# Kernel optimization log

Hardware: AMD Instinct MI355X
Metric: run time of the kernel (lower is better)

Reference implementation:

```python
import jax, jax.numpy as jnp
import numpy as np

INPUT_SIZE = 1024
OUTPUT_SIZE = 1024
HEADS = 8
FREQ = 10000.0
NEG_INF = -1e9


def absolute_position(T, d, freq):
    # AP[p, 2i] = sin(p / freq^(2i/d)); AP[p, 2i+1] = cos(...). T assumed even.
    pos = jnp.arange(T, dtype=jnp.float32)[:, None]          # [T, 1]
    i = jnp.arange(T // 2, dtype=jnp.float32)[None, :]       # [1, T//2]
    angle = pos / (freq ** (2.0 * i / d))                    # [T, T//2]
    return jnp.stack([jnp.sin(angle), jnp.cos(angle)], axis=-1).reshape(T, T)


def setup_inputs() -> dict:
    key = jax.random.key(0)
    k_x, k_m, k_q, k_k, k_v, k_o = jax.random.split(key, 6)
    bs, n = 4, 2048
    dh = OUTPUT_SIZE // HEADS
    s_in = 1.0 / np.sqrt(INPUT_SIZE)
    s_out = 1.0 / np.sqrt(OUTPUT_SIZE)
    return {
        "x": jax.random.normal(k_x, (bs, n, INPUT_SIZE), dtype=jnp.float32),
        "mask": jax.random.randint(k_m, (bs, n), 0, 2, dtype=jnp.int32),
        # torch Linear weight layout: [out_features, in_features], stacked per head -> [H, dh, D]
        "Wq": jax.random.uniform(k_q, (HEADS, dh, INPUT_SIZE), jnp.float32, -s_in, s_in),
        "Wk": jax.random.uniform(k_k, (HEADS, dh, INPUT_SIZE), jnp.float32, -s_in, s_in),
        "Wv": jax.random.uniform(k_v, (HEADS, dh, INPUT_SIZE), jnp.float32, -s_in, s_in),
        "Wout": jax.random.uniform(k_o, (INPUT_SIZE, OUTPUT_SIZE), jnp.float32, -s_out, s_out),
    }


def reference(x, mask, Wq, Wk, Wv, Wout):
    bs, n, d = x.shape
    # per-head projections (no bias): [b, h, n, dh]
    Q = jnp.einsum('bnd,hed->bhne', x, Wq)
    K = jnp.einsum('bnd,hed->bhne', x, Wk)
    V = jnp.einsum('bnd,hed->bhne', x, Wv)
    # unscaled scores, as in the original module
    energies = jnp.einsum('bhqe,bhke->bhqk', Q, K)             # [b, h, n, n]
    AP = absolute_position(n, d, FREQ)                         # [n, n]
    energies = energies + AP
    m = mask.astype(bool)
    attn_mask = m[:, None, :, None] & m[:, None, None, :]      # [b, 1, n, n]
    energies = jnp.where(attn_mask, energies, NEG_INF)
    A = jax.nn.softmax(energies, axis=-1)                      # [b, h, n, n]
    # original computes (V^T @ A)^T == A^T @ V  (note transposed attention)
    y = jnp.einsum('bhji,bhje->bhie', A, V)                    # [b, h, n, dh]
    y = y.transpose(0, 2, 1, 3).reshape(bs, n, -1)             # concat heads -> [b, n, D]
    out = jnp.einsum('bnd,od->bno', y, Wout)
    return out, A[:, -1]  # original returns last head's att_weights
```

## Files before the change

### kernel.cpp

```cpp
#include <hip/hip_runtime.h>
#include <math.h>

#define BS_ 4
#define N_  2048
#define D_  1024
#define H_  8
#define DH_ 128

typedef __attribute__((ext_vector_type(8))) short short8;
typedef __attribute__((ext_vector_type(4))) short short4_t;
typedef __attribute__((ext_vector_type(4))) float float4_t;
typedef unsigned short u16;

__device__ __forceinline__ u16 f2bf(float f) {
    union { float f; unsigned u; } v; v.f = f;
    unsigned r = v.u + 0x7FFFu + ((v.u >> 16) & 1u);
    return (u16)(r >> 16);
}
__device__ __forceinline__ float bf2f(u16 h) {
    union { unsigned u; float f; } v; v.u = ((unsigned)h) << 16;
    return v.f;
}
__device__ __forceinline__ void split4(float a, float b, float c, float d,
                                       short4_t* hi, short4_t* lo) {
    u16 h0 = f2bf(a), h1 = f2bf(b), h2 = f2bf(c), h3 = f2bf(d);
    (*hi)[0] = (short)h0; (*hi)[1] = (short)h1; (*hi)[2] = (short)h2; (*hi)[3] = (short)h3;
    (*lo)[0] = (short)f2bf(a - bf2f(h0));
    (*lo)[1] = (short)f2bf(b - bf2f(h1));
    (*lo)[2] = (short)f2bf(c - bf2f(h2));
    (*lo)[3] = (short)f2bf(d - bf2f(h3));
}

__device__ __forceinline__ void gl_lds16(const void* g, void* l) {
    __builtin_amdgcn_global_load_lds(
        (const __attribute__((address_space(1))) unsigned int*)g,
        (__attribute__((address_space(3))) unsigned int*)l,
        16, 0, 0);
}

__global__ void apt_kernel(unsigned int* __restrict__ APtw) {
    int idx = blockIdx.x * 256 + threadIdx.x;
    int i = idx >> 10;
    int jw = idx & 1023;
    int u = i >> 1;
    float ex = exp2f(-(float)u * (13.287712379549449f / 512.0f));
    float a0 = (float)(2 * jw) * ex;
    float a1 = (float)(2 * jw + 1) * ex;
    float v0, v1;
    if (i & 1) { v0 = cosf(a0); v1 = cosf(a1); }
    else       { v0 = sinf(a0); v1 = sinf(a1); }
    APtw[(size_t)i * (N_ / 2) + jw] = (unsigned)f2bf(v0) | ((unsigned)f2bf(v1) << 16);
}

__global__ void split_kernel(const float* __restrict__ x,
                             const float* __restrict__ Wq, const float* __restrict__ Wk,
                             const float* __restrict__ Wv, const float* __restrict__ Wo,
                             u16* __restrict__ Xhi, u16* __restrict__ Xlo,
                             u16* __restrict__ Whi, u16* __restrict__ Wlo,
                             u16* __restrict__ Wvhi, u16* __restrict__ Wohi) {
    int i = blockIdx.x * 256 + threadIdx.x;
    const float* src; u16 *dhi, *dlo; size_t off;
    if (i < 2097152)      { src = x  + 4*(size_t)i;             dhi = Xhi;  dlo = Xlo;  off = 4*(size_t)i; }
    else if (i < 2359296) { size_t j = i - 2097152; src = Wq + 4*j; dhi = Whi; dlo = Wlo; off = 4*j; }
    else if (i < 2621440) { size_t j = i - 2359296; src = Wk + 4*j; dhi = Whi; dlo = Wlo; off = 1048576 + 4*j; }
    else if (i < 2883584) { size_t j = i - 2621440; src = Wv + 4*j; dhi = Wvhi; dlo = nullptr; off = 4*j; }
    else                  { size_t j = i - 2883584; src = Wo + 4*j; dhi = Wohi; dlo = nullptr; off = 4*j; }
    float4 v = *(const float4*)src;
    short4_t hi, lo;
    split4(v.x, v.y, v.z, v.w, &hi, &lo);
    *(short4_t*)(dhi + off) = hi;
    if (dlo) *(short4_t*)(dlo + off) = lo;
}

__global__ __launch_bounds__(256, 4) void qk_gemm(
    const u16* __restrict__ Xhi, const u16* __restrict__ Xlo,
    const u16* __restrict__ Whi, const u16* __restrict__ Wlo,
    u16* __restrict__ Qhi, u16* __restrict__ Qlo,
    u16* __restrict__ Khi, u16* __restrict__ Klo)
{
    const int mt = blockIdx.x;
    const int nt = blockIdx.y;
    const int tid = threadIdx.x, wave = tid >> 6, lane = tid & 63;
    const int quad = lane >> 4, l16 = lane & 15;

    __shared__ __align__(16) u16 sA[2][128 * 32];
    __shared__ __align__(16) u16 sB[2][128 * 32];

    const int srow = lane >> 2;
    const int scol = (lane & 3) * 8;
    const size_t aoff = ((size_t)(mt * 128) + srow) * 1024 + scol;
    const size_t boff = ((size_t)(nt * 128) + srow) * 1024 + scol;
    const int r0 = wave * 16, r1 = 64 + wave * 16;

    float4_t acc[2][8];
#pragma unroll
    for (int i = 0; i < 2; ++i)
#pragma unroll
        for (int j = 0; j < 8; ++j) acc[i][j] = (float4_t)(0.f);

    for (int kt = 0; kt < 32; ++kt) {
        __syncthreads();
        const int kc0 = kt * 32;
        gl_lds16(Xhi + aoff + (size_t)r0 * 1024 + kc0, &sA[0][r0 * 32]);
        gl_lds16(Xhi + aoff + (size_t)r1 * 1024 + kc0, &sA[0][r1 * 32]);
        gl_lds16(Xlo + aoff + (size_t)r0 * 1024 + kc0, &sA[1][r0 * 32]);
        gl_lds16(Xlo + aoff + (size_t)r1 * 1024 + kc0, &sA[1][r1 * 32]);
        gl_lds16(Whi + boff + (size_t)r0 * 1024 + kc0, &sB[0][r0 * 32]);
        gl_lds16(Whi + boff + (size_t)r1 * 1024 + kc0, &sB[0][r1 * 32]);
        gl_lds16(Wlo + boff + (size_t)r0 * 1024 + kc0, &sB[1][r0 * 32]);
        gl_lds16(Wlo + boff + (size_t)r1 * 1024 + kc0, &sB[1][r1 * 32]);
        __syncthreads();

#pragma unroll
        for (int t = 0; t < 3; ++t) {
            const u16* As = sA[t == 2 ? 1 : 0];
            const u16* Bs = sB[t == 1 ? 1 : 0];
            short8 afr[2];
#pragma unroll
            for (int mi = 0; mi < 2; ++mi)
                afr[mi] = *(const short8*)(As + (wave * 32 + mi * 16 + l16) * 32 + quad * 8);
#pragma unroll
            for (int ne = 0; ne < 8; ++ne) {
                short8 bfr = *(const short8*)(Bs + (ne * 16 + l16) * 32 + quad * 8);
#pragma unroll
                for (int mi = 0; mi < 2; ++mi)
                    acc[mi][ne] = __builtin_amdgcn_mfma_f32_16x16x32_bf16(afr[mi], bfr, acc[mi][ne], 0, 0, 0);
            }
        }
    }

    const int b = mt >> 4, q0 = (mt & 15) * 128;
    const bool isQ = (nt < 8);
    u16* Hi = isQ ? Qhi : Khi;
    u16* Lo = isQ ? Qlo : Klo;
    const int h = isQ ? nt : nt - 8;
    const size_t base = (size_t)(b * 8 + h) * N_ * DH_;
#pragma unroll
    for (int mi = 0; mi < 2; ++mi)
#pragma unroll
        for (int ne = 0; ne < 8; ++ne)
#pragma unroll
            for (int r = 0; r < 4; ++r) {
                int q = q0 + wave * 32 + mi * 16 + quad * 4 + r;
                int e = ne * 16 + l16;
                float v = acc[mi][ne][r];
                u16 hv = f2bf(v);
                Hi[base + (size_t)q * DH_ + e] = hv;
                Lo[base + (size_t)q * DH_ + e] = f2bf(v - bf2f(hv));
            }
}

__global__ __launch_bounds__(256, 4) void v_gemm(
    const u16* __restrict__ Wvhi, const u16* __restrict__ Xhi,
    u16* __restrict__ VT)
{
    const int qt = blockIdx.x;
    const int bh = blockIdx.y;
    const int b = bh >> 3, h = bh & 7;
    const int tid = threadIdx.x, wave = tid >> 6, lane = tid & 63;
    const int quad = lane >> 4, l16 = lane & 15;

    __shared__ __align__(16) u16 sA[128 * 32];
    __shared__ __align__(16) u16 sB[128 * 32];

    const int srow = lane >> 2, scol = (lane & 3) * 8;
    const size_t aoff = ((size_t)(h * 128) + srow) * 1024 + scol;
    const size_t boff = ((size_t)(b * N_ + qt * 128) + srow) * 1024 + scol;
    const int r0 = wave * 16, r1 = 64 + wave * 16;

    float4_t acc[2][8];
#pragma unroll
    for (int i = 0; i < 2; ++i)
#pragma unroll
        for (int j = 0; j < 8; ++j) acc[i][j] = (float4_t)(0.f);

    for (int kt = 0; kt < 32; ++kt) {
        __syncthreads();
        const int kc0 = kt * 32;
        gl_lds16(Wvhi + aoff + (size_t)r0 * 1024 + kc0, &sA[r0 * 32]);
        gl_lds16(Wvhi + aoff + (size_t)r1 * 1024 + kc0, &sA[r1 * 32]);
        gl_lds16(Xhi  + boff + (size_t)r0 * 1024 + kc0, &sB[r0 * 32]);
        gl_lds16(Xhi  + boff + (size_t)r1 * 1024 + kc0, &sB[r1 * 32]);
        __syncthreads();

        short8 afr[2];
#pragma unroll
        for (int mi = 0; mi < 2; ++mi)
            afr[mi] = *(const short8*)(sA + (wave * 32 + mi * 16 + l16) * 32 + quad * 8);
#pragma unroll
        for (int ne = 0; ne < 8; ++ne) {
            short8 bfr = *(const short8*)(sB + (ne * 16 + l16) * 32 + quad * 8);
#pragma unroll
            for (int mi = 0; mi < 2; ++mi)
                acc[mi][ne] = __builtin_amdgcn_mfma_f32_16x16x32_bf16(afr[mi], bfr, acc[mi][ne], 0, 0, 0);
        }
    }

    u16* Cg = VT + (size_t)bh * DH_ * N_;
#pragma unroll
    for (int mi = 0; mi < 2; ++mi)
#pragma unroll
        for (int ne = 0; ne < 8; ++ne)
#pragma unroll
            for (int r = 0; r < 4; ++r) {
                int e = wave * 32 + mi * 16 + quad * 4 + r;
                int q = qt * 128 + ne * 16 + l16;
                Cg[(size_t)e * N_ + q] = f2bf(acc[mi][ne][r]);
            }
}

__global__ __launch_bounds__(512, 4) void rowstats_kernel(
    const u16* __restrict__ Qhi, const u16* __restrict__ Qlo,
    const u16* __restrict__ Khi, const u16* __restrict__ Klo,
    const u16* __restrict__ APt,
    const int* __restrict__ mask,
    float* __restrict__ lrow)
{
    const int jt = blockIdx.x;
    const int bh = blockIdx.y;
    const int b = bh >> 3;
    const int tid = threadIdx.x, wave = tid >> 6, lane = tid & 63;
    const int quad = lane >> 4, l16 = lane & 15;
    const int jsub = (wave & 3) * 16, khalf = wave >> 2;

    __shared__ __align__(16) u16 ldsK[2][64 * 264];
    __shared__ int   s_mk[2][64];
    __shared__ float psum[64 * 2];

    short8 rQh[4], rQl[4];
    {
        const size_t qrow = ((size_t)bh * N_ + (size_t)(jt * 64 + jsub + l16)) * DH_;
#pragma unroll
        for (int kc = 0; kc < 4; ++kc) {
            rQh[kc] = *(const short8*)(Qhi + qrow + kc * 32 + quad * 8);
            rQl[kc] = *(const short8*)(Qlo + qrow + kc * 32 + quad * 8);
        }
    }

    const u16* ap_base = APt + (size_t)(khalf * 32 + l16) * N_ + jt * 64 + jsub + quad * 4;
    short4_t apc[2];
#pragma unroll
    for (int nk = 0; nk < 2; ++nk)
        apc[nk] = *(const short4_t*)(ap_base + (size_t)(nk * 16) * N_);

    {
        const size_t Kb = ((size_t)bh * N_) * DH_;
        for (int c = tid; c < 2048; c += 512) {
            int row = c >> 5, half = (c >> 4) & 1, seg = c & 15;
            *(short8*)(ldsK[0] + row * 264 + half * 128 + seg * 8) =
                *(const short8*)((half ? Klo : Khi) + Kb + (size_t)row * DH_ + seg * 8);
        }
        if (tid < 64) s_mk[0][tid] = mask[b * N_ + tid];
    }

    float p[4] = {0.f, 0.f, 0.f, 0.f};
    int mj_on[4];
#pragma unroll
    for (int r = 0; r < 4; ++r)
        mj_on[r] = mask[b * N_ + jt * 64 + jsub + quad * 4 + r];

    __syncthreads();

    for (int kt = 0; kt < 32; ++kt) {
        const int cur = kt & 1, nxt = cur ^ 1;
        short8 rK[4];
        short4_t apn[2];
        int rmk = 0;
        if (kt < 31) {
            const size_t Kb2 = ((size_t)bh * N_ + (size_t)(kt + 1) * 64) * DH_;
#pragma unroll
            for (int i = 0; i < 4; ++i) {
                int c = tid + i * 512;
                int row = c >> 5, half = (c >> 4) & 1, seg = c & 15;
                rK[i] = *(const short8*)((half ? Klo : Khi) + Kb2 + (size_t)row * DH_ + seg * 8);
            }
#pragma unroll
            for (int nk = 0; nk < 2; ++nk)
                apn[nk] = *(const short4_t*)(ap_base + (size_t)((kt + 1) * 64 + nk * 16) * N_);
            if (tid < 64) rmk = mask[b * N_ + (kt + 1) * 64 + tid];
        }

        float4_t acc[2];
        acc[0] = (float4_t)(0.f); acc[1] = (float4_t)(0.f);
#pragma unroll
        for (int kc = 0; kc < 4; ++kc) {
            short8 bH[2], bL[2];
#pragma unroll
            for (int nk = 0; nk < 2; ++nk)
                bH[nk] = *(const short8*)(ldsK[cur] + (khalf * 32 + nk * 16 + l16) * 264 + kc * 32 + quad * 8);
#pragma unroll
            for (int nk = 0; nk < 2; ++nk)
                acc[nk] = __builtin_amdgcn_mfma_f32_16x16x32_bf16(rQh[kc], bH[nk], acc[nk], 0, 0, 0);
#pragma unroll
            for (int nk = 0; nk < 2; ++nk)
                acc[nk] = __builtin_amdgcn_mfma_f32_16x16x32_bf16(rQl[kc], bH[nk], acc[nk], 0, 0, 0);
#pragma unroll
            for (int nk = 0; nk < 2; ++nk)
                bL[nk] = *(const short8*)(ldsK[cur] + (khalf * 32 + nk * 16 + l16) * 264 + 128 + kc * 32 + quad * 8);
#pragma unroll
            for (int nk = 0; nk < 2; ++nk)
                acc[nk] = __builtin_amdgcn_mfma_f32_16x16x32_bf16(rQh[kc], bL[nk], acc[nk], 0, 0, 0);
        }

#pragma unroll
        for (int nk = 0; nk < 2; ++nk) {
            int kk = khalf * 32 + nk * 16 + l16;
            int mk = s_mk[cur][kk];
#pragma unroll
            for (int r = 0; r < 4; ++r) {
                float e = acc[nk][r] + bf2f((u16)apc[nk][r]);
                e = (mj_on[r] && mk) ? e : -1.0e9f;
                p[r] += __expf(e);
            }
        }

        if (kt < 31) {
#pragma unroll
            for (int i = 0; i < 4; ++i) {
                int c = tid + i * 512;
                int row = c >> 5, half = (c >> 4) & 1, seg = c & 15;
                *(short8*)(ldsK[nxt] + row * 264 + half * 128 + seg * 8) = rK[i];
            }
            if (tid < 64) s_mk[nxt][tid] = rmk;
            apc[0] = apn[0]; apc[1] = apn[1];
        }
        __syncthreads();
    }

#pragma unroll
    for (int r = 0; r < 4; ++r) {
        float s = p[r];
        for (int off = 1; off < 16; off <<= 1)
            s += __shfl_xor(s, off, 64);
        if (l16 == 0)
            psum[(jsub + quad * 4 + r) * 2 + khalf] = s;
    }
    __syncthreads();
    if (tid < 64)
        lrow[(size_t)bh * N_ + jt * 64 + tid] = psum[tid * 2] + psum[tid * 2 + 1];
}

__global__ __launch_bounds__(512, 4) void attn_kernel(
    const u16* __restrict__ Qhi, const u16* __restrict__ Qlo,
    const u16* __restrict__ Khi, const u16* __restrict__ Klo,
    const u16* __restrict__ VT,
    const u16* __restrict__ APt,
    const int* __restrict__ mask,
    const float* __restrict__ lrow,
    u16* __restrict__ yout,
    float* __restrict__ aout)
{
    const int it = blockIdx.x;
    const int bh = blockIdx.y;
    const int b = bh >> 3, h = bh & 7;
    const int tid = threadIdx.x, wave = tid >> 6, lane = tid & 63;
    const int quad = lane >> 4, l16 = lane & 15;

    __shared__ __align__(16) u16 ldsQ[2][32 * 264];
    __shared__ __align__(16) u16 ldsV[2][128 * 40];
    __shared__ __align__(16) u16 ldsA[128 * 40];
    __shared__ float s_il[2][32];
    __shared__ int   s_dead[2][32];
    __shared__ int   s_mj[2][32];

    const int i_local = wave * 16 + l16;
    const int ig = it * 128 + i_local;

    short8 rKh[4], rKl[4];
    {
        const size_t krow = ((size_t)bh * N_ + ig) * DH_;
#pragma unroll
        for (int kc = 0; kc < 4; ++kc) {
            rKh[kc] = *(const short8*)(Khi + krow + kc * 32 + quad * 8);
            rKl[kc] = *(const short8*)(Klo + krow + kc * 32 + quad * 8);
        }
    }

    const u16* ap_base = APt + (size_t)ig * N_ + quad * 4;
    short4_t apc[2];
#pragma unroll
    for (int mj = 0; mj < 2; ++mj)
        apc[mj] = *(const short4_t*)(ap_base + mj * 16);

    {
        const size_t Qb0 = ((size_t)bh * N_) * DH_;
        for (int c = tid; c < 1024; c += 512) {
            int row = c >> 5, half = (c >> 4) & 1, seg = c & 15;
            *(short8*)(ldsQ[0] + row * 264 + half * 128 + seg * 8) =
                *(const short8*)((half ? Qlo : Qhi) + Qb0 + (size_t)row * DH_ + seg * 8);
        }
        { int e = tid >> 2, seg = tid & 3;
          *(short8*)(ldsV[0] + e * 40 + seg * 8) =
              *(const short8*)(VT + (size_t)bh * DH_ * N_ + (size_t)e * N_ + seg * 8); }
        if (tid < 32) {
            float l = lrow[(size_t)bh * N_ + tid];
            int mj = mask[b * N_ + tid];
            int alive = (mj != 0) && (l > 0.f);
            s_il[0][tid] = alive ? 1.0f / l : 0.f;
            s_dead[0][tid] = !alive;
            s_mj[0][tid] = mj;
        }
    }

    const int ion = mask[b * N_ + ig];
    const int ip = wave >> 1, eh = wave & 1;

    float4_t accy[2][4];
#pragma unroll
    for (int ni = 0; ni < 2; ++ni)
#pragma unroll
        for (int ne = 0; ne < 4; ++ne) accy[ni][ne] = (float4_t)(0.f);

    const bool do_aout = (h == 7);
    const float inv_n = 1.0f / (float)N_;

    __syncthreads();

    for (int jt = 0; jt < 64; ++jt) {
        const int cur = jt & 1, nxt = cur ^ 1;
        const int j0 = jt * 32;

        short8 rQ[2], rV;
        short4_t apn[2];
        float r_il = 0.f; int r_dead = 0, r_mj = 0;
        if (jt < 63) {
            const int j0n = j0 + 32;
            const size_t Qb2 = ((size_t)bh * N_ + j0n) * DH_;
#pragma unroll
            for (int i = 0; i < 2; ++i) {
                int c = tid + i * 512;
                int row = c >> 5, half = (c >> 4) & 1, seg = c & 15;
                rQ[i] = *(const short8*)((half ? Qlo : Qhi) + Qb2 + (size_t)row * DH_ + seg * 8);
            }
            { int e = tid >> 2, seg = tid & 3;
              rV = *(const short8*)(VT + (size_t)bh * DH_ * N_ + (size_t)e * N_ + j0n + seg * 8); }
#pragma unroll
            for (int mj = 0; mj < 2; ++mj)
                apn[mj] = *(const short4_t*)(ap_base + j0n + mj * 16);
            if (tid < 32) {
                float l = lrow[(size_t)bh * N_ + j0n + tid];
                r_mj = mask[b * N_ + j0n + tid];
                int alive = (r_mj != 0) && (l > 0.f);
                r_il = alive ? 1.0f / l : 0.f;
                r_dead = !alive;
            }
        }

        float4_t accs[2];
        accs[0] = (float4_t)(0.f); accs[1] = (float4_t)(0.f);
#pragma unroll
        for (int kc = 0; kc < 4; ++kc) {
            short8 aH[2], aL[2];
#pragma unroll
            for (int mj = 0; mj < 2; ++mj)
                aH[mj] = *(const short8*)(ldsQ[cur] + (mj * 16 + l16) * 264 + kc * 32 + quad * 8);
#pragma unroll
            for (int mj = 0; mj < 2; ++mj)
                accs[mj] = __builtin_amdgcn_mfma_f32_16x16x32_bf16(aH[mj], rKh[kc], accs[mj], 0, 0, 0);
#pragma unroll
            for (int mj = 0; mj < 2; ++mj)
                aL[mj] = *(const short8*)(ldsQ[cur] + (mj * 16 + l16) * 264 + 128 + kc * 32 + quad * 8);
#pragma unroll
            for (int mj = 0; mj < 2; ++mj)
                accs[mj] = __builtin_amdgcn_mfma_f32_16x16x32_bf16(aL[mj], rKh[kc], accs[mj], 0, 0, 0);
#pragma unroll
            for (int mj = 0; mj < 2; ++mj)
                accs[mj] = __builtin_amdgcn_mfma_f32_16x16x32_bf16(aH[mj], rKl[kc], accs[mj], 0, 0, 0);
        }

#pragma unroll
        for (int mj = 0; mj < 2; ++mj) {
            short4_t pk;
#pragma unroll
            for (int r = 0; r < 4; ++r) {
                int jl = mj * 16 + quad * 4 + r;
                float e = accs[mj][r] + bf2f((u16)apc[mj][r]);
                e = (s_mj[cur][jl] && ion) ? e : -1.0e9f;
                float a = s_dead[cur][jl] ? inv_n : __expf(e) * s_il[cur][jl];
                pk[r] = (short)f2bf(a);
                if (do_aout)
                    aout[((size_t)(b * N_ + j0 + jl)) * N_ + ig] = a;
            }
            *(short4_t*)(ldsA + (size_t)i_local * 40 + mj * 16 + quad * 4) = pk;
        }
        __syncthreads();

        {
            short8 afrA[2];
#pragma unroll
            for (int ni = 0; ni < 2; ++ni)
                afrA[ni] = *(const short8*)(ldsA + (ip * 32 + ni * 16 + l16) * 40 + quad * 8);
#pragma unroll
            for (int ne = 0; ne < 4; ++ne) {
                short8 bfr = *(const short8*)(ldsV[cur] + (eh * 64 + ne * 16 + l16) * 40 + quad * 8);
#pragma unroll
                for (int ni = 0; ni < 2; ++ni)
                    accy[ni][ne] = __builtin_amdgcn_mfma_f32_16x16x32_bf16(afrA[ni], bfr, accy[ni][ne], 0, 0, 0);
            }
        }

        if (jt < 63) {
#pragma unroll
            for (int i = 0; i < 2; ++i) {
                int c = tid + i * 512;
                int row = c >> 5, half = (c >> 4) & 1, seg = c & 15;
                *(short8*)(ldsQ[nxt] + row * 264 + half * 128 + seg * 8) = rQ[i];
            }
            { int e = tid >> 2, seg = tid & 3;
              *(short8*)(ldsV[nxt] + e * 40 + seg * 8) = rV; }
            if (tid < 32) {
                s_il[nxt][tid] = r_il;
                s_dead[nxt][tid] = r_dead;
                s_mj[nxt][tid] = r_mj;
            }
            apc[0] = apn[0]; apc[1] = apn[1];
        }
        __syncthreads();
    }

#pragma unroll
    for (int ni = 0; ni < 2; ++ni)
#pragma unroll
        for (int ne = 0; ne < 4; ++ne)
#pragma unroll
            for (int r = 0; r < 4; ++r) {
                int irow = ip * 32 + ni * 16 + quad * 4 + r;
                int e = eh * 64 + ne * 16 + l16;
                yout[((size_t)b * N_ + it * 128 + irow) * D_ + h * DH_ + e] =
                    f2bf(accy[ni][ne][r]);
            }
}

__global__ __launch_bounds__(256, 4) void outgemm_kernel(
    const u16* __restrict__ A,
    const u16* __restrict__ B,
    float* __restrict__ C)
{
    const int nt = blockIdx.x;
    const int mt = blockIdx.y;
    const int tid = threadIdx.x, wave = tid >> 6, lane = tid & 63;
    const int quad = lane >> 4, l16 = lane & 15;

    __shared__ __align__(16) u16 sA[128 * 32];
    __shared__ __align__(16) u16 sB[128 * 32];

    const int srow = lane >> 2, scol = (lane & 3) * 8;
    const size_t aoff = ((size_t)(mt * 128) + srow) * 1024 + scol;
    const size_t boff = ((size_t)(nt * 128) + srow) * 1024 + scol;
    const int r0 = wave * 16, r1 = 64 + wave * 16;

    float4_t acc[2][8];
#pragma unroll
    for (int i = 0; i < 2; ++i)
#pragma unroll
        for (int j = 0; j < 8; ++j) acc[i][j] = (float4_t)(0.f);

    for (int kt = 0; kt < 32; ++kt) {
        __syncthreads();
        const int kc0 = kt * 32;
        gl_lds16(A + aoff + (size_t)r0 * 1024 + kc0, &sA[r0 * 32]);
        gl_lds16(A + aoff + (size_t)r1 * 1024 + kc0, &sA[r1 * 32]);
        gl_lds16(B + boff + (size_t)r0 * 1024 + kc0, &sB[r0 * 32]);
        gl_lds16(B + boff + (size_t)r1 * 1024 + kc0, &sB[r1 * 32]);
        __syncthreads();

        short8 afr[2];
#pragma unroll
        for (int mi = 0; mi < 2; ++mi)
            afr[mi] = *(const short8*)(sA + (wave * 32 + mi * 16 + l16) * 32 + quad * 8);
#pragma unroll
        for (int ne = 0; ne < 8; ++ne) {
            short8 bfr = *(const short8*)(sB + (ne * 16 + l16) * 32 + quad * 8);
#pragma unroll
            for (int mi = 0; mi < 2; ++mi)
                acc[mi][ne] = __builtin_amdgcn_mfma_f32_16x16x32_bf16(afr[mi], bfr, acc[mi][ne], 0, 0, 0);
        }
    }

#pragma unroll
    for (int mi = 0; mi < 2; ++mi)
#pragma unroll
        for (int ne = 0; ne < 8; ++ne)
#pragma unroll
            for (int r = 0; r < 4; ++r) {
                int row = mt * 128 + wave * 32 + mi * 16 + quad * 4 + r;
                int col = nt * 128 + ne * 16 + l16;
                C[(size_t)row * D_ + col] = acc[mi][ne][r];
            }
}

extern "C" void kernel_launch(void* const* d_in, const int* in_sizes, int n_in,
                              void* d_out, int out_size, void* d_ws, size_t ws_size,
                              hipStream_t stream)
{
    const float* x   = (const float*)d_in[0];
    const int*   msk = (const int*)d_in[1];
    const float* Wq  = (const float*)d_in[2];
    const float* Wk  = (const float*)d_in[3];
    const float* Wv  = (const float*)d_in[4];
    const float* Wo  = (const float*)d_in[5];

    float* out  = (float*)d_out;
    float* aout = out + (size_t)BS_ * N_ * D_;

    u16* Whi  = (u16*)d_out;
    u16* Wlo  = Whi  + (size_t)2048 * 1024;
    u16* Wvhi = Wlo  + (size_t)2048 * 1024;
    u16* Xhi  = Wvhi + (size_t)1024 * 1024;
    u16* Xlo  = Xhi  + (size_t)8192 * 1024;

    char* w = (char*)d_ws;
    u16* APt = (u16*)w;                       w += (size_t)N_ * N_ * 2;
    const size_t szqk = (size_t)BS_ * H_ * N_ * DH_ * 2;
    u16* Qhi = (u16*)w; w += szqk;
    u16* Qlo = (u16*)w; w += szqk;
    u16* Khi = (u16*)w; w += szqk;
    u16* Klo = (u16*)w; w += szqk;
    u16* VT  = (u16*)w; w += szqk;
    float* lrow = (float*)w;                  w += (size_t)BS_ * H_ * N_ * 4;
    u16* Wohi = (u16*)w;                      w += (size_t)D_ * D_ * 2;
    u16* yb   = (u16*)w;                      w += (size_t)BS_ * N_ * D_ * 2;

    apt_kernel<<<8192, 256, 0, stream>>>((unsigned int*)APt);
    split_kernel<<<12288, 256, 0, stream>>>(x, Wq, Wk, Wv, Wo,
                                            Xhi, Xlo, Whi, Wlo, Wvhi, Wohi);
    qk_gemm<<<dim3(64, 16), 256, 0, stream>>>(Xhi, Xlo, Whi, Wlo,
                                              Qhi, Qlo, Khi, Klo);
    v_gemm<<<dim3(16, 32), 256, 0, stream>>>(Wvhi, Xhi, VT);
    rowstats_kernel<<<dim3(32, 32), 512, 0, stream>>>(Qhi, Qlo, Khi, Klo, APt, msk, lrow);
    attn_kernel<<<dim3(16, 32), 512, 0, stream>>>(Qhi, Qlo, Khi, Klo, VT, APt, msk,
                                                  lrow, yb, aout);
    outgemm_kernel<<<dim3(8, 64), 256, 0, stream>>>(yb, Wohi, out);
}
```

Before: 683.1 us.

## Retile score phase per wave, async-load V to LDS, pack mask/inv-l into one table

Each wave now computes scores for 32 i-rows by 16 j-columns instead of 16 i-rows by 32 j-columns. Each Q LDS fragment is reused across two K register fragments, which halves the Q LDS reads but doubles the K registers held per thread. V tiles go from global straight into LDS through a gl_lds16 helper with an unpadded stride of 32, removing the register staging. The three per-column tables (inverse l, dead flag, mask) are packed into one float array that uses a negative sentinel, and launch bounds drop from 4 to 3 waves per SIMD to allow more registers. The unpadded V layout may cause LDS bank conflicts, and the lower occupancy target may reduce latency hiding.

```diff
diff --git a/kernel.cpp b/kernel.cpp
--- a/kernel.cpp
+++ b/kernel.cpp
@@ -340,7 +340,7 @@
         lrow[(size_t)bh * N_ + jt * 64 + tid] = psum[tid * 2] + psum[tid * 2 + 1];
 }
 
-__global__ __launch_bounds__(512, 4) void attn_kernel(
+__global__ __launch_bounds__(512, 3) void attn_kernel(
     const u16* __restrict__ Qhi, const u16* __restrict__ Qlo,
     const u16* __restrict__ Khi, const u16* __restrict__ Klo,
     const u16* __restrict__ VT,
@@ -357,30 +357,35 @@
     const int quad = lane >> 4, l16 = lane & 15;
 
     __shared__ __align__(16) u16 ldsQ[2][32 * 264];
-    __shared__ __align__(16) u16 ldsV[2][128 * 40];
+    __shared__ __align__(16) u16 ldsV[2][128 * 32];
     __shared__ __align__(16) u16 ldsA[128 * 40];
-    __shared__ float s_il[2][32];
-    __shared__ int   s_dead[2][32];
-    __shared__ int   s_mj[2][32];
-
-    const int i_local = wave * 16 + l16;
-    const int ig = it * 128 + i_local;
-
-    short8 rKh[4], rKl[4];
+    __shared__ __align__(16) float s_g[2][32];
+
+    const int iq = wave & 3, jh = wave >> 2;
+    const int igv0 = it * 128 + iq * 32 + l16;
+    const int igv1 = igv0 + 16;
+
+    short8 rKh[4][2], rKl[4][2];
     {
-        const size_t krow = ((size_t)bh * N_ + ig) * DH_;
+        const size_t kr0 = ((size_t)bh * N_ + igv0) * DH_;
+        const size_t kr1 = ((size_t)bh * N_ + igv1) * DH_;
 #pragma unroll
         for (int kc = 0; kc < 4; ++kc) {
-            rKh[kc] = *(const short8*)(Khi + krow + kc * 32 + quad * 8);
-            rKl[kc] = *(const short8*)(Klo + krow + kc * 32 + quad * 8);
-        }
-    }
-
-    const u16* ap_base = APt + (size_t)ig * N_ + quad * 4;
+            rKh[kc][0] = *(const short8*)(Khi + kr0 + kc * 32 + quad * 8);
+            rKh[kc][1] = *(const short8*)(Khi + kr1 + kc * 32 + quad * 8);
+            rKl[kc][0] = *(const short8*)(Klo + kr0 + kc * 32 + quad * 8);
+            rKl[kc][1] = *(const short8*)(Klo + kr1 + kc * 32 + quad * 8);
+        }
+    }
+
+    const u16* apb0 = APt + (size_t)igv0 * N_ + jh * 16 + quad * 4;
+    const u16* apb1 = APt + (size_t)igv1 * N_ + jh * 16 + quad * 4;
     short4_t apc[2];
-#pragma unroll
-    for (int mj = 0; mj < 2; ++mj)
-        apc[mj] = *(const short4_t*)(ap_base + mj * 16);
+    apc[0] = *(const short4_t*)(apb0);
+    apc[1] = *(const short4_t*)(apb1);
+
+    const int ion0 = mask[b * N_ + igv0];
+    const int ion1 = mask[b * N_ + igv1];
 
     {
         const size_t Qb0 = ((size_t)bh * N_) * DH_;
@@ -390,19 +395,15 @@
                 *(const short8*)((half ? Qlo : Qhi) + Qb0 + (size_t)row * DH_ + seg * 8);
         }
         { int e = tid >> 2, seg = tid & 3;
-          *(short8*)(ldsV[0] + e * 40 + seg * 8) =
-              *(const short8*)(VT + (size_t)bh * DH_ * N_ + (size_t)e * N_ + seg * 8); }
+          gl_lds16(VT + (size_t)bh * DH_ * N_ + (size_t)e * N_ + seg * 8,
+                   &ldsV[0][wave * 512]); }
         if (tid < 32) {
             float l = lrow[(size_t)bh * N_ + tid];
             int mj = mask[b * N_ + tid];
-            int alive = (mj != 0) && (l > 0.f);
-            s_il[0][tid] = alive ? 1.0f / l : 0.f;
-            s_dead[0][tid] = !alive;
-            s_mj[0][tid] = mj;
-        }
-    }
-
-    const int ion = mask[b * N_ + ig];
+            s_g[0][tid] = (mj && l > 0.f) ? 1.0f / l : -1.0f;
+        }
+    }
+
     const int ip = wave >> 1, eh = wave & 1;
 
     float4_t accy[2][4];
@@ -420,11 +421,14 @@
         const int cur = jt & 1, nxt = cur ^ 1;
         const int j0 = jt * 32;
 
-        short8 rQ[2], rV;
+        short8 rQ[2];
         short4_t apn[2];
-        float r_il = 0.f; int r_dead = 0, r_mj = 0;
+        float r_g = 0.f;
         if (jt < 63) {
             const int j0n = j0 + 32;
+            { int e = tid >> 2, seg = tid & 3;
+              gl_lds16(VT + (size_t)bh * DH_ * N_ + (size_t)e * N_ + j0n + seg * 8,
+                       &ldsV[nxt][wave * 512]); }
             const size_t Qb2 = ((size_t)bh * N_ + j0n) * DH_;
 #pragma unroll
             for (int i = 0; i < 2; ++i) {
@@ -432,56 +436,49 @@
                 int row = c >> 5, half = (c >> 4) & 1, seg = c & 15;
                 rQ[i] = *(const short8*)((half ? Qlo : Qhi) + Qb2 + (size_t)row * DH_ + seg * 8);
             }
-            { int e = tid >> 2, seg = tid & 3;
-              rV = *(const short8*)(VT + (size_t)bh * DH_ * N_ + (size_t)e * N_ + j0n + seg * 8); }
-#pragma unroll
-            for (int mj = 0; mj < 2; ++mj)
-                apn[mj] = *(const short4_t*)(ap_base + j0n + mj * 16);
+            apn[0] = *(const short4_t*)(apb0 + j0n);
+            apn[1] = *(const short4_t*)(apb1 + j0n);
             if (tid < 32) {
                 float l = lrow[(size_t)bh * N_ + j0n + tid];
-                r_mj = mask[b * N_ + j0n + tid];
-                int alive = (r_mj != 0) && (l > 0.f);
-                r_il = alive ? 1.0f / l : 0.f;
-                r_dead = !alive;
+                int mj = mask[b * N_ + j0n + tid];
+                r_g = (mj && l > 0.f) ? 1.0f / l : -1.0f;
             }
         }
 
         float4_t accs[2];
         accs[0] = (float4_t)(0.f); accs[1] = (float4_t)(0.f);
+        const u16* qbase = ldsQ[cur] + (jh * 16 + l16) * 264 + quad * 8;
 #pragma unroll
         for (int kc = 0; kc < 4; ++kc) {
-            short8 aH[2], aL[2];
-#pragma unroll
-            for (int mj = 0; mj < 2; ++mj)
-                aH[mj] = *(const short8*)(ldsQ[cur] + (mj * 16 + l16) * 264 + kc * 32 + quad * 8);
-#pragma unroll
-            for (int mj = 0; mj < 2; ++mj)
-                accs[mj] = __builtin_amdgcn_mfma_f32_16x16x32_bf16(aH[mj], rKh[kc], accs[mj], 0, 0, 0);
-#pragma unroll
-            for (int mj = 0; mj < 2; ++mj)
-                aL[mj] = *(const short8*)(ldsQ[cur] + (mj * 16 + l16) * 264 + 128 + kc * 32 + quad * 8);
-#pragma unroll
-            for (int mj = 0; mj < 2; ++mj)
-                accs[mj] = __builtin_amdgcn_mfma_f32_16x16x32_bf16(aL[mj], rKh[kc], accs[mj], 0, 0, 0);
-#pragma unroll
-            for (int mj = 0; mj < 2; ++mj)
-                accs[mj] = __builtin_amdgcn_mfma_f32_16x16x32_bf16(aH[mj], rKl[kc], accs[mj], 0, 0, 0);
-        }
-
-#pragma unroll
-        for (int mj = 0; mj < 2; ++mj) {
-            short4_t pk;
-#pragma unroll
-            for (int r = 0; r < 4; ++r) {
-                int jl = mj * 16 + quad * 4 + r;
-                float e = accs[mj][r] + bf2f((u16)apc[mj][r]);
-                e = (s_mj[cur][jl] && ion) ? e : -1.0e9f;
-                float a = s_dead[cur][jl] ? inv_n : __expf(e) * s_il[cur][jl];
-                pk[r] = (short)f2bf(a);
-                if (do_aout)
-                    aout[((size_t)(b * N_ + j0 + jl)) * N_ + ig] = a;
-            }
-            *(short4_t*)(ldsA + (size_t)i_local * 40 + mj * 16 + quad * 4) = pk;
+            short8 aH = *(const short8*)(qbase + kc * 32);
+            accs[0] = __builtin_amdgcn_mfma_f32_16x16x32_bf16(aH, rKh[kc][0], accs[0], 0, 0, 0);
+            accs[1] = __builtin_amdgcn_mfma_f32_16x16x32_bf16(aH, rKh[kc][1], accs[1], 0, 0, 0);
+            short8 aL = *(const short8*)(qbase + 128 + kc * 32);
+            accs[0] = __builtin_amdgcn_mfma_f32_16x16x32_bf16(aL, rKh[kc][0], accs[0], 0, 0, 0);
+            accs[1] = __builtin_amdgcn_mfma_f32_16x16x32_bf16(aL, rKh[kc][1], accs[1], 0, 0, 0);
+            accs[0] = __builtin_amdgcn_mfma_f32_16x16x32_bf16(aH, rKl[kc][0], accs[0], 0, 0, 0);
+            accs[1] = __builtin_amdgcn_mfma_f32_16x16x32_bf16(aH, rKl[kc][1], accs[1], 0, 0, 0);
+        }
+
+        {
+            float4_t g4 = *(const float4_t*)(&s_g[cur][jh * 16 + quad * 4]);
+#pragma unroll
+            for (int ih = 0; ih < 2; ++ih) {
+                const int ig = ih ? igv1 : igv0;
+                const int ion = ih ? ion1 : ion0;
+                short4_t pk;
+#pragma unroll
+                for (int r = 0; r < 4; ++r) {
+                    int jl = jh * 16 + quad * 4 + r;
+                    float e = accs[ih][r] + bf2f((u16)apc[ih][r]);
+                    float g = g4[r];
+                    float a = (g < 0.f) ? inv_n : (ion ? __expf(e) * g : 0.f);
+                    pk[r] = (short)f2bf(a);
+                    if (do_aout)
+                        aout[((size_t)(b * N_ + j0 + jl)) * N_ + ig] = a;
+                }
+                *(short4_t*)(ldsA + (size_t)(iq * 32 + ih * 16 + l16) * 40 + jh * 16 + quad * 4) = pk;
+            }
         }
         __syncthreads();
 
@@ -492,7 +489,7 @@
                 afrA[ni] = *(const short8*)(ldsA + (ip * 32 + ni * 16 + l16) * 40 + quad * 8);
 #pragma unroll
             for (int ne = 0; ne < 4; ++ne) {
-                short8 bfr = *(const short8*)(ldsV[cur] + (eh * 64 + ne * 16 + l16) * 40 + quad * 8);
+                short8 bfr = *(const short8*)(ldsV[cur] + (eh * 64 + ne * 16 + l16) * 32 + quad * 8);
 #pragma unroll
                 for (int ni = 0; ni < 2; ++ni)
                     accy[ni][ne] = __builtin_amdgcn_mfma_f32_16x16x32_bf16(afrA[ni], bfr, accy[ni][ne], 0, 0, 0);
@@ -506,13 +503,7 @@
                 int row = c >> 5, half = (c >> 4) & 1, seg = c & 15;
                 *(short8*)(ldsQ[nxt] + row * 264 + half * 128 + seg * 8) = rQ[i];
             }
-            { int e = tid >> 2, seg = tid & 3;
-              *(short8*)(ldsV[nxt] + e * 40 + seg * 8) = rV; }
-            if (tid < 32) {
-                s_il[nxt][tid] = r_il;
-                s_dead[nxt][tid] = r_dead;
-                s_mj[nxt][tid] = r_mj;
-            }
+            if (tid < 32) s_g[nxt][tid] = r_g;
             apc[0] = apn[0]; apc[1] = apn[1];
         }
         __syncthreads();
```

Result: no change. 673.6 us (-1.4%).
